# Performance work log

Hardware: AMD Instinct MI355X
Metric: run time of the kernel (lower is better)

## Reference

```python
import jax, jax.numpy as jnp
import numpy as np

H = W = 224
NSR = NSC = 8          # num_segments_row / col
BW = 5                 # band_width (default of adjust_boundaries)
K = NSR * NSC          # 64 superpixels
B = 256


def find_paths(g, inits, bw):
    """Seam-carving DP along axis 0 of g. g: (L, M); inits: (P,) start columns.
    Returns optimal paths (P, L) of column indices per row."""
    L, M = g.shape
    P = inits.shape[0]
    idx_pos = jnp.clip(inits[:, None] + jnp.arange(-bw, bw + 1)[None, :], 0, M - 1)  # (P, Np)
    Np = idx_pos.shape[1]
    C = -g[:, idx_pos]  # (L, P, Np) unary cost per row
    neigh = jnp.clip(jnp.arange(Np)[:, None] + jnp.array([-1, 0, 1])[None, :], 0, Np - 1)  # (Np,3)
    pos = jnp.arange(Np)
    r = jnp.arange(P)

    def step(cost_prev, c_y):
        padded = jnp.pad(cost_prev, ((0, 0), (1, 1)), constant_values=jnp.inf)  # (P, Np+2)
        prev_costs = padded[:, neigh + 1]                                        # (P, Np, 3)
        min_prev = prev_costs.min(axis=-1)
        min_idx = prev_costs.argmin(axis=-1)          # first-min, matches torch .min
        path_y = neigh[pos[None, :], min_idx]          # (P, Np) backpointers
        return min_prev + c_y, path_y

    cost_last, path_arr = jax.lax.scan(step, C[0], C[1:])  # path_arr: (L-1, P, Np)
    idx = jnp.argmin(cost_last, axis=1)                    # (P,)

    def back(idx, p_y):
        out = idx_pos[r, idx]
        return p_y[r, idx], out

    idx0, outs = jax.lax.scan(back, idx, path_arr, reverse=True)  # outs: (L-1, P) for y=1..L-1
    out0 = idx_pos[r, idx0]
    paths = jnp.concatenate([out0[None], outs], axis=0)  # (L, P)
    return paths.T


def segment_image(g):
    """g: (H, W) gradient map -> (H, W) int32 segmentation labels."""
    x_inits = jnp.clip(jnp.arange(1, NSC) * (W // NSC), 0, W - 1)
    y_inits = jnp.clip(jnp.arange(1, NSR) * (H // NSR), 0, H - 1)
    vpaths = find_paths(g, x_inits, BW)      # (7, H): column index per row
    hpaths = find_paths(g.T, y_inits, BW)    # (7, W): row index per column
    rows = jnp.broadcast_to(jnp.arange(H), vpaths.shape)
    cols = jnp.broadcast_to(jnp.arange(W), hpaths.shape)
    vmask = jnp.zeros((H, W), jnp.int32).at[rows, vpaths].set(1)
    hmask = jnp.zeros((H, W), jnp.int32).at[hpaths, cols].set(1)
    vlab = jnp.cumsum(vmask, axis=1)   # vertical label in [0, 7]
    hlab = jnp.cumsum(hmask, axis=0)   # horizontal label in [0, 7]
    return vlab + NSC * hlab           # labels in [0, 63]


def centroids_of(mask):
    flat = mask.reshape(-1)
    yc = jnp.repeat(jnp.arange(H, dtype=jnp.float32), W)
    xc = jnp.tile(jnp.arange(W, dtype=jnp.float32), H)
    sy = jax.ops.segment_sum(yc, flat, num_segments=K)
    sx = jax.ops.segment_sum(xc, flat, num_segments=K)
    cnt = jnp.maximum(jax.ops.segment_sum(jnp.ones_like(yc), flat, num_segments=K), 1e-6)
    return jnp.stack([sy / cnt, sx / cnt], axis=-1)  # (K, 2) [y, x]


def setup_inputs() -> dict:
    key = jax.random.key(0)
    k1, k2 = jax.random.split(key)
    x = jax.random.normal(k1, (B, 3, H, W), dtype=jnp.float32)
    grad_map = jax.random.uniform(k2, (B, H, W), dtype=jnp.float32)
    return {"x": x, "grad_map": grad_map}


def reference(x, grad_map):
    masks = jax.vmap(segment_image)(grad_map)          # (B, H, W) int32
    cents = jax.vmap(centroids_of)(masks)              # (B, K, 2) float32
    return cents, masks.astype(jnp.int64)
```

## Files before the change

### kernel.cpp

```cpp
#include <hip/hip_runtime.h>
#include <stdint.h>

#define HH 224
#define WW 224
#define NSEAM 7
#define BWIDTH 5
#define BB 256
#define KK 64
#define YCH 8
#define YROWS (HH / YCH)

#define DPPF_OLD(old, src, ctrl) \
    __int_as_float(__builtin_amdgcn_update_dpp(__float_as_int(old), __float_as_int(src), ctrl, 0xF, 0xF, false))
#define DPPF_Z(src, ctrl) \
    __int_as_float(__builtin_amdgcn_update_dpp(0, __float_as_int(src), ctrl, 0xF, 0xF, true))
#define DPPI_Z(src, ctrl) \
    __builtin_amdgcn_update_dpp(0, (int)(src), ctrl, 0xF, 0xF, true)

__global__ __launch_bounds__(256) void dp_kernel(const float* __restrict__ g,
                                                 int* __restrict__ paths,
                                                 unsigned long long* __restrict__ gacc) {
    __shared__ uint32_t ch[16][226];
    __shared__ int      pth[16][226];

    {
        int t = blockIdx.x * 256 + threadIdx.x;
        if (t < BB * KK) gacc[t] = 0ull;
    }

    const int j   = threadIdx.x & 15;
    const int grp = threadIdx.x >> 4;
    const int gid = blockIdx.x * 16 + grp;
    const int dir = gid / (BB * NSEAM);
    const int rem = gid - dir * (BB * NSEAM);
    const int b   = rem / NSEAM;
    const int p   = rem - b * NSEAM;
    const int band0 = 28 * (p + 1) - BWIDTH;
    const int jc  = (j > 10) ? 10 : j;
    const float* gb  = g + (size_t)b * HH * WW;
    const float* gp0 = gb + band0 + jc;
    const float* gp1 = gb + (size_t)(band0 + jc) * WW;
    const unsigned isj0 = (j == 0) ? 1u : 0u;

    float bufA[16], bufB[16], cost;

#define LOADC(BUF, c)                                                       \
    if (dir == 0) {                                                         \
        _Pragma("unroll")                                                   \
        for (int rr = 0; rr < 16; ++rr) BUF[rr] = gp0[((c) * 16 + rr) * WW];\
    } else {                                                                \
        const float4* q4 = reinterpret_cast<const float4*>(gp1 + (c) * 16); \
        float4 t0 = q4[0], t1 = q4[1], t2 = q4[2], t3 = q4[3];              \
        BUF[0] = t0.x;  BUF[1] = t0.y;  BUF[2] = t0.z;  BUF[3] = t0.w;      \
        BUF[4] = t1.x;  BUF[5] = t1.y;  BUF[6] = t1.z;  BUF[7] = t1.w;      \
        BUF[8] = t2.x;  BUF[9] = t2.y;  BUF[10] = t2.z; BUF[11] = t2.w;     \
        BUF[12] = t3.x; BUF[13] = t3.y; BUF[14] = t3.z; BUF[15] = t3.w;     \
    }

#define ROWSEL(BUF, rr)                                                     \
    {                                                                       \
        float pm  = DPPF_OLD(cost, cost, 0x111);                            \
        float pv  = DPPF_OLD(cost, cost, 0x101);                            \
        pv = (j >= 10) ? cost : pv;                                         \
        float best = fminf(fminf(pm, cost), pv);                            \
        unsigned cc = (cost == best) ? 1u : 0u;                             \
        unsigned b0 = (pm == best) ? isj0 : cc;                             \
        unsigned b1 = (pm == best) ? 0u : (cc ^ 1u);                        \
        cost = best - (BUF)[rr];                                            \
        selLo |= b0 << (rr);                                                \
        selHi |= b1 << (rr);                                                \
    }

#define TR16(x)                                                             \
    {                                                                       \
        unsigned pp;                                                        \
        pp = (unsigned)__builtin_amdgcn_ds_swizzle((int)(x), 0x201F);       \
        x = (j & 8) ? ((x & 0xFF00u) | ((pp >> 8) & 0x00FFu))               \
                    : ((x & 0x00FFu) | ((pp << 8) & 0xFF00u));              \
        pp = (unsigned)__builtin_amdgcn_ds_swizzle((int)(x), 0x101F);       \
        x = (j & 4) ? ((x & 0xF0F0u) | ((pp >> 4) & 0x0F0Fu))               \
                    : ((x & 0x0F0Fu) | ((pp << 4) & 0xF0F0u));              \
        pp = (unsigned)__builtin_amdgcn_ds_swizzle((int)(x), 0x081F);       \
        x = (j & 2) ? ((x & 0xCCCCu) | ((pp >> 2) & 0x3333u))               \
                    : ((x & 0x3333u) | ((pp << 2) & 0xCCCCu));              \
        pp = (unsigned)__builtin_amdgcn_ds_swizzle((int)(x), 0x041F);       \
        x = (j & 1) ? ((x & 0xAAAAu) | ((pp >> 1) & 0x5555u))               \
                    : ((x & 0x5555u) | ((pp << 1) & 0xAAAAu));              \
    }

#define PROCC(BUF, c)                                                       \
    {                                                                       \
        unsigned selLo = 0u, selHi = 0u;                                    \
        _Pragma("unroll")                                                   \
        for (int rr = 0; rr < 16; ++rr) ROWSEL(BUF, rr)                     \
        TR16(selLo)                                                         \
        TR16(selHi)                                                         \
        ch[grp][(c) * 16 + j] = selLo | (selHi << 16);                      \
    }

    LOADC(bufA, 0);
    LOADC(bufB, 1);
    {
        unsigned selLo = 0u, selHi = 0u;
        cost = -bufA[0];
#pragma unroll
        for (int rr = 1; rr < 16; ++rr) ROWSEL(bufA, rr)
        TR16(selLo)
        TR16(selHi)
        ch[grp][j] = selLo | (selHi << 16);
    }
    LOADC(bufA, 2);
    PROCC(bufB, 1);
    LOADC(bufB, 3);

#pragma unroll 1
    for (int c2 = 2; c2 <= 12; c2 += 2) {
        PROCC(bufA, c2);
        if (c2 + 2 < 14) LOADC(bufA, c2 + 2);
        PROCC(bufB, c2 + 1);
        if (c2 + 3 < 14) LOADC(bufB, c2 + 3);
    }

    float rc = (j <= 10) ? cost : INFINITY;
    int   ri = (j <= 10) ? j : 15;
#define REDSTEP(ctrl)                                                        \
    {                                                                        \
        float oc = DPPF_Z(rc, ctrl);                                         \
        int   oi = DPPI_Z(ri, ctrl);                                         \
        bool t = (oc < rc) || (oc == rc && oi < ri);                         \
        rc = t ? oc : rc; ri = t ? oi : ri;                                  \
    }
    REDSTEP(0x128) REDSTEP(0x124) REDSTEP(0x122) REDSTEP(0x121)
#undef REDSTEP

    int pos = ri;
    if (j == 0) pth[grp][HH - 1] = band0 + pos;

#pragma unroll 1
    for (int c = 13; c >= 0; --c) {
        uint32_t w[16];
#pragma unroll
        for (int rr = 0; rr < 16; ++rr) w[rr] = ch[grp][c * 16 + rr];
#pragma unroll
        for (int rr = 15; rr >= 0; --rr) {
            int r = c * 16 + rr;
            if (r >= 1) {
                uint32_t ww = w[rr];
                int sel = (int)((ww >> pos) & 1u) | (int)((ww >> (pos + 15)) & 2u);
                pos += sel - 1;
                if (j == 0) pth[grp][r - 1] = band0 + pos;
            }
        }
    }

    int* op = paths + (size_t)(b * 14 + dir * NSEAM + p) * HH;
#pragma unroll 1
    for (int c = 0; c < 14; ++c) op[c * 16 + j] = pth[grp][c * 16 + j];

#undef LOADC
#undef ROWSEL
#undef TR16
#undef PROCC
}

__global__ __launch_bounds__(256) void label_kernel(const int* __restrict__ paths,
                                                    float* __restrict__ out,
                                                    unsigned long long* __restrict__ gacc) {
    const int b  = blockIdx.x >> 3;
    const int cy = blockIdx.x & 7;
    const int y0 = cy * YROWS;

    __shared__ unsigned char vpc[NSEAM][YROWS];
    __shared__ unsigned long long acc[KK];

    const int* pb = paths + (size_t)b * 14 * HH;
    for (int i = threadIdx.x; i < NSEAM * YROWS; i += 256) {
        int q = i / YROWS, r = i - q * YROWS;
        vpc[q][r] = (unsigned char)pb[q * HH + y0 + r];
    }
    if (threadIdx.x < KK) acc[threadIdx.x] = 0ull;
    __syncthreads();

    const int x = threadIdx.x;
    if (x < WW) {
        int basev = 0, kv = 0, inv = 0;
        if (x >= 23) {
            int q = x - 23, k = q / 28, r = q - k * 28;
            if (k > 6) basev = 7;
            else { inv = (r <= 10) ? 1 : 0; basev = k + (r > 10 ? 1 : 0); kv = k; }
        }
        const int hA = (cy >= 1) ? pb[(NSEAM + cy - 1) * HH + x] : 0;
        const int hB = (cy <= 6) ? pb[(NSEAM + cy) * HH + x] : 0;

        float* mb = out + (size_t)BB * KK * 2 + (size_t)b * HH * WW + x;
        int cur = -1, ys = y0;

#define FLUSH(yend)                                                          \
        {                                                                    \
            unsigned cnt = (unsigned)((yend) - ys);                          \
            unsigned sy  = (unsigned)((ys + (yend) - 1) * ((yend) - ys) / 2);\
            unsigned sx  = (unsigned)x * cnt;                                \
            atomicAdd(&acc[cur], ((unsigned long long)cnt << 42) |           \
                                 ((unsigned long long)sy << 21) |            \
                                 (unsigned long long)sx);                    \
        }
#define ROW(t, HLEXPR)                                                       \
        {                                                                    \
            const int y = y0 + (t);                                          \
            int vl = basev + ((inv && (int)vpc[kv][t] <= x) ? 1 : 0);        \
            int lab = vl + 8 * (HLEXPR);                                     \
            mb[y * WW] = (float)lab;                                         \
            if (lab != cur) { if (cur >= 0) FLUSH(y); cur = lab; ys = y; }   \
        }
#pragma unroll
        for (int t = 0; t < 6; ++t)
            ROW(t, (cy >= 1) ? (cy - 1 + ((hA <= y0 + t) ? 1 : 0)) : 0)
#pragma unroll
        for (int t = 6; t < 23; ++t)
            ROW(t, cy)
#pragma unroll
        for (int t = 23; t < 28; ++t)
            ROW(t, (cy <= 6) ? (cy + ((hB <= y0 + t) ? 1 : 0)) : 7)
        FLUSH(y0 + YROWS)
#undef ROW
#undef FLUSH
    }
    __syncthreads();

    if (threadIdx.x < KK) {
        unsigned long long v = acc[threadIdx.x];
        if (v) atomicAdd(&gacc[(size_t)b * KK + threadIdx.x], v);
    }
}

__global__ __launch_bounds__(256) void finalize_kernel(const unsigned long long* __restrict__ gacc,
                                                       float* __restrict__ out) {
    int i = blockIdx.x * 256 + threadIdx.x;
    unsigned long long sv = gacc[i];
    float cnt = (float)(unsigned)(sv >> 42);
    float sy  = (float)(unsigned)((sv >> 21) & 0x1FFFFFu);
    float sx  = (float)(unsigned)(sv & 0x1FFFFFu);
    float c = fmaxf(cnt, 1e-6f);
    float2 r; r.x = sy / c; r.y = sx / c;
    *reinterpret_cast<float2*>(out + (size_t)i * 2) = r;
}

extern "C" void kernel_launch(void* const* d_in, const int* in_sizes, int n_in,
                              void* d_out, int out_size, void* d_ws, size_t ws_size,
                              hipStream_t stream) {
    const float* g = (const float*)d_in[1];
    float* out = (float*)d_out;
    int* paths = (int*)d_ws;
    unsigned long long* gacc =
        (unsigned long long*)((char*)d_ws + (size_t)BB * 14 * HH * 4);

    dp_kernel<<<(BB * 14) / 16, 256, 0, stream>>>(g, paths, gacc);
    label_kernel<<<BB * YCH, 256, 0, stream>>>(paths, out, gacc);
    finalize_kernel<<<(BB * KK) / 256, 256, 0, stream>>>(gacc, out);
}
```

Before: 45.52 us.

## Fuse DP, labeling and centroid finalize into one per-image kernel

Replaces three launches (seam DP, label/atomic accumulation, finalize) with one 1024-thread block per image. Seam paths stay in shared memory as bytes, and centroids are finalized from shared accumulators, so the global paths buffer, global atomics and two launches go away. In exchange only 256 blocks run, and during the DP phase just 224 of the 1024 threads are busy while the rest wait at the barrier. This cuts parallelism compared with the previous 224-block DP plus 2048-block label grid.

```diff
diff --git a/kernel.cpp b/kernel.cpp
--- a/kernel.cpp
+++ b/kernel.cpp
@@ -7,8 +7,6 @@
 #define BWIDTH 5
 #define BB 256
 #define KK 64
-#define YCH 8
-#define YROWS (HH / YCH)
 
 #define DPPF_OLD(old, src, ctrl) \
     __int_as_float(__builtin_amdgcn_update_dpp(__float_as_int(old), __float_as_int(src), ctrl, 0xF, 0xF, false))
@@ -17,32 +15,30 @@
 #define DPPI_Z(src, ctrl) \
     __builtin_amdgcn_update_dpp(0, (int)(src), ctrl, 0xF, 0xF, true)
 
-__global__ __launch_bounds__(256) void dp_kernel(const float* __restrict__ g,
-                                                 int* __restrict__ paths,
-                                                 unsigned long long* __restrict__ gacc) {
-    __shared__ uint32_t ch[16][226];
-    __shared__ int      pth[16][226];
-
-    {
-        int t = blockIdx.x * 256 + threadIdx.x;
-        if (t < BB * KK) gacc[t] = 0ull;
-    }
-
-    const int j   = threadIdx.x & 15;
-    const int grp = threadIdx.x >> 4;
-    const int gid = blockIdx.x * 16 + grp;
-    const int dir = gid / (BB * NSEAM);
-    const int rem = gid - dir * (BB * NSEAM);
-    const int b   = rem / NSEAM;
-    const int p   = rem - b * NSEAM;
-    const int band0 = 28 * (p + 1) - BWIDTH;
-    const int jc  = (j > 10) ? 10 : j;
-    const float* gb  = g + (size_t)b * HH * WW;
-    const float* gp0 = gb + band0 + jc;
-    const float* gp1 = gb + (size_t)(band0 + jc) * WW;
-    const unsigned isj0 = (j == 0) ? 1u : 0u;
-
-    float bufA[16], bufB[16], cost;
+__global__ __launch_bounds__(1024) void fused_kernel(const float* __restrict__ g,
+                                                     float* __restrict__ out) {
+    __shared__ uint32_t ch[14][226];
+    __shared__ unsigned char pv8[HH][8];
+    __shared__ unsigned char ph8[8][HH];
+    __shared__ unsigned long long acc[KK];
+
+    const int tid = threadIdx.x;
+    const int b   = blockIdx.x;
+    if (tid < KK) acc[tid] = 0ull;
+
+    if (tid < 14 * 16) {
+        const int j    = tid & 15;
+        const int grp  = tid >> 4;
+        const int dir  = grp / 7;
+        const int p    = grp % 7;
+        const int band0 = 28 * (p + 1) - BWIDTH;
+        const int jc   = (j > 10) ? 10 : j;
+        const float* gb  = g + (size_t)b * HH * WW;
+        const float* gp0 = gb + band0 + jc;
+        const float* gp1 = gb + (size_t)(band0 + jc) * WW;
+        const unsigned isj0 = (j == 0) ? 1u : 0u;
+
+        float bufA[16], bufB[16], cost;
 
 #define LOADC(BUF, c)                                                       \
     if (dir == 0) {                                                         \
@@ -98,90 +94,76 @@
         ch[grp][(c) * 16 + j] = selLo | (selHi << 16);                      \
     }
 
-    LOADC(bufA, 0);
-    LOADC(bufB, 1);
-    {
-        unsigned selLo = 0u, selHi = 0u;
-        cost = -bufA[0];
-#pragma unroll
-        for (int rr = 1; rr < 16; ++rr) ROWSEL(bufA, rr)
-        TR16(selLo)
-        TR16(selHi)
-        ch[grp][j] = selLo | (selHi << 16);
-    }
-    LOADC(bufA, 2);
-    PROCC(bufB, 1);
-    LOADC(bufB, 3);
+        LOADC(bufA, 0);
+        LOADC(bufB, 1);
+        {
+            unsigned selLo = 0u, selHi = 0u;
+            cost = -bufA[0];
+#pragma unroll
+            for (int rr = 1; rr < 16; ++rr) ROWSEL(bufA, rr)
+            TR16(selLo)
+            TR16(selHi)
+            ch[grp][j] = selLo | (selHi << 16);
+        }
+        LOADC(bufA, 2);
+        PROCC(bufB, 1);
+        LOADC(bufB, 3);
 
 #pragma unroll 1
-    for (int c2 = 2; c2 <= 12; c2 += 2) {
-        PROCC(bufA, c2);
-        if (c2 + 2 < 14) LOADC(bufA, c2 + 2);
-        PROCC(bufB, c2 + 1);
-        if (c2 + 3 < 14) LOADC(bufB, c2 + 3);
-    }
-
-    float rc = (j <= 10) ? cost : INFINITY;
-    int   ri = (j <= 10) ? j : 15;
+        for (int c2 = 2; c2 <= 12; c2 += 2) {
+            PROCC(bufA, c2);
+            if (c2 + 2 < 14) LOADC(bufA, c2 + 2);
+            PROCC(bufB, c2 + 1);
+            if (c2 + 3 < 14) LOADC(bufB, c2 + 3);
+        }
+
+        float rc = (j <= 10) ? cost : INFINITY;
+        int   ri = (j <= 10) ? j : 15;
 #define REDSTEP(ctrl)                                                        \
-    {                                                                        \
-        float oc = DPPF_Z(rc, ctrl);                                         \
-        int   oi = DPPI_Z(ri, ctrl);                                         \
-        bool t = (oc < rc) || (oc == rc && oi < ri);                         \
-        rc = t ? oc : rc; ri = t ? oi : ri;                                  \
-    }
-    REDSTEP(0x128) REDSTEP(0x124) REDSTEP(0x122) REDSTEP(0x121)
+        {                                                                    \
+            float oc = DPPF_Z(rc, ctrl);                                     \
+            int   oi = DPPI_Z(ri, ctrl);                                     \
+            bool t = (oc < rc) || (oc == rc && oi < ri);                     \
+            rc = t ? oc : rc; ri = t ? oi : ri;                              \
+        }
+        REDSTEP(0x128) REDSTEP(0x124) REDSTEP(0x122) REDSTEP(0x121)
 #undef REDSTEP
 
-    int pos = ri;
-    if (j == 0) pth[grp][HH - 1] = band0 + pos;
+        int pos = ri;
+        const bool wr = (j == 0);
+        if (wr) {
+            if (dir == 0) pv8[HH - 1][p] = (unsigned char)(band0 + pos);
+            else          ph8[p][HH - 1] = (unsigned char)(band0 + pos);
+        }
 
 #pragma unroll 1
-    for (int c = 13; c >= 0; --c) {
-        uint32_t w[16];
-#pragma unroll
-        for (int rr = 0; rr < 16; ++rr) w[rr] = ch[grp][c * 16 + rr];
-#pragma unroll
-        for (int rr = 15; rr >= 0; --rr) {
-            int r = c * 16 + rr;
-            if (r >= 1) {
-                uint32_t ww = w[rr];
-                int sel = (int)((ww >> pos) & 1u) | (int)((ww >> (pos + 15)) & 2u);
-                pos += sel - 1;
-                if (j == 0) pth[grp][r - 1] = band0 + pos;
+        for (int c = 13; c >= 0; --c) {
+            uint32_t w[16];
+#pragma unroll
+            for (int rr = 0; rr < 16; ++rr) w[rr] = ch[grp][c * 16 + rr];
+#pragma unroll
+            for (int rr = 15; rr >= 0; --rr) {
+                int r = c * 16 + rr;
+                if (r >= 1) {
+                    uint32_t ww = w[rr];
+                    int sel = (int)((ww >> pos) & 1u) | (int)((ww >> (pos + 15)) & 2u);
+                    pos += sel - 1;
+                    if (wr) {
+                        if (dir == 0) pv8[r - 1][p] = (unsigned char)(band0 + pos);
+                        else          ph8[p][r - 1] = (unsigned char)(band0 + pos);
+                    }
+                }
             }
         }
-    }
-
-    int* op = paths + (size_t)(b * 14 + dir * NSEAM + p) * HH;
-#pragma unroll 1
-    for (int c = 0; c < 14; ++c) op[c * 16 + j] = pth[grp][c * 16 + j];
-
 #undef LOADC
 #undef ROWSEL
 #undef TR16
 #undef PROCC
-}
-
-__global__ __launch_bounds__(256) void label_kernel(const int* __restrict__ paths,
-                                                    float* __restrict__ out,
-                                                    unsigned long long* __restrict__ gacc) {
-    const int b  = blockIdx.x >> 3;
-    const int cy = blockIdx.x & 7;
-    const int y0 = cy * YROWS;
-
-    __shared__ unsigned char vpc[NSEAM][YROWS];
-    __shared__ unsigned long long acc[KK];
-
-    const int* pb = paths + (size_t)b * 14 * HH;
-    for (int i = threadIdx.x; i < NSEAM * YROWS; i += 256) {
-        int q = i / YROWS, r = i - q * YROWS;
-        vpc[q][r] = (unsigned char)pb[q * HH + y0 + r];
-    }
-    if (threadIdx.x < KK) acc[threadIdx.x] = 0ull;
+    }
+
     __syncthreads();
 
-    const int x = threadIdx.x;
+    const int x = tid & 255;
     if (x < WW) {
         int basev = 0, kv = 0, inv = 0;
         if (x >= 23) {
@@ -189,60 +171,58 @@
             if (k > 6) basev = 7;
             else { inv = (r <= 10) ? 1 : 0; basev = k + (r > 10 ? 1 : 0); kv = k; }
         }
-        const int hA = (cy >= 1) ? pb[(NSEAM + cy - 1) * HH + x] : 0;
-        const int hB = (cy <= 6) ? pb[(NSEAM + cy) * HH + x] : 0;
-
         float* mb = out + (size_t)BB * KK * 2 + (size_t)b * HH * WW + x;
-        int cur = -1, ys = y0;
+
+#pragma unroll
+        for (int ov = 0; ov < 2; ++ov) {
+            const int cy = (tid >> 8) + 4 * ov;
+            const int y0 = cy * 28;
+            const int hA = (cy >= 1) ? (int)ph8[cy - 1][x] : 0;
+            const int hB = (cy <= 6) ? (int)ph8[cy][x] : 0;
+            int cur = -1, ys = y0;
 
 #define FLUSH(yend)                                                          \
-        {                                                                    \
-            unsigned cnt = (unsigned)((yend) - ys);                          \
-            unsigned sy  = (unsigned)((ys + (yend) - 1) * ((yend) - ys) / 2);\
-            unsigned sx  = (unsigned)x * cnt;                                \
-            atomicAdd(&acc[cur], ((unsigned long long)cnt << 42) |           \
-                                 ((unsigned long long)sy << 21) |            \
-                                 (unsigned long long)sx);                    \
-        }
+            {                                                                \
+                unsigned cnt = (unsigned)((yend) - ys);                      \
+                unsigned sy  = (unsigned)((ys + (yend) - 1) * ((yend) - ys) / 2);\
+                unsigned sx  = (unsigned)x * cnt;                            \
+                atomicAdd(&acc[cur], ((unsigned long long)cnt << 42) |       \
+                                     ((unsigned long long)sy << 21) |        \
+                                     (unsigned long long)sx);                \
+            }
 #define ROW(t, HLEXPR)                                                       \
-        {                                                                    \
-            const int y = y0 + (t);                                          \
-            int vl = basev + ((inv && (int)vpc[kv][t] <= x) ? 1 : 0);        \
-            int lab = vl + 8 * (HLEXPR);                                     \
-            mb[y * WW] = (float)lab;                                         \
-            if (lab != cur) { if (cur >= 0) FLUSH(y); cur = lab; ys = y; }   \
-        }
-#pragma unroll
-        for (int t = 0; t < 6; ++t)
-            ROW(t, (cy >= 1) ? (cy - 1 + ((hA <= y0 + t) ? 1 : 0)) : 0)
-#pragma unroll
-        for (int t = 6; t < 23; ++t)
-            ROW(t, cy)
-#pragma unroll
-        for (int t = 23; t < 28; ++t)
-            ROW(t, (cy <= 6) ? (cy + ((hB <= y0 + t) ? 1 : 0)) : 7)
-        FLUSH(y0 + YROWS)
+            {                                                                \
+                const int y = y0 + (t);                                      \
+                int vl = basev + ((inv && (int)pv8[y][kv] <= x) ? 1 : 0);    \
+                int lab = vl + 8 * (HLEXPR);                                 \
+                mb[y * WW] = (float)lab;                                     \
+                if (lab != cur) { if (cur >= 0) FLUSH(y); cur = lab; ys = y; }\
+            }
+#pragma unroll
+            for (int t = 0; t < 6; ++t)
+                ROW(t, (cy >= 1) ? (cy - 1 + ((hA <= y0 + t) ? 1 : 0)) : 0)
+#pragma unroll
+            for (int t = 6; t < 23; ++t)
+                ROW(t, cy)
+#pragma unroll
+            for (int t = 23; t < 28; ++t)
+                ROW(t, (cy <= 6) ? (cy + ((hB <= y0 + t) ? 1 : 0)) : 7)
+            FLUSH(y0 + 28)
 #undef ROW
 #undef FLUSH
+        }
     }
     __syncthreads();
 
-    if (threadIdx.x < KK) {
-        unsigned long long v = acc[threadIdx.x];
-        if (v) atomicAdd(&gacc[(size_t)b * KK + threadIdx.x], v);
-    }
-}
-
-__global__ __launch_bounds__(256) void finalize_kernel(const unsigned long long* __restrict__ gacc,
-                                                       float* __restrict__ out) {
-    int i = blockIdx.x * 256 + threadIdx.x;
-    unsigned long long sv = gacc[i];
-    float cnt = (float)(unsigned)(sv >> 42);
-    float sy  = (float)(unsigned)((sv >> 21) & 0x1FFFFFu);
-    float sx  = (float)(unsigned)(sv & 0x1FFFFFu);
-    float c = fmaxf(cnt, 1e-6f);
-    float2 r; r.x = sy / c; r.y = sx / c;
-    *reinterpret_cast<float2*>(out + (size_t)i * 2) = r;
+    if (tid < KK) {
+        unsigned long long sv = acc[tid];
+        float cnt = (float)(unsigned)(sv >> 42);
+        float sy  = (float)(unsigned)((sv >> 21) & 0x1FFFFFu);
+        float sx  = (float)(unsigned)(sv & 0x1FFFFFu);
+        float c = fmaxf(cnt, 1e-6f);
+        float2 r; r.x = sy / c; r.y = sx / c;
+        *reinterpret_cast<float2*>(out + (size_t)b * KK * 2 + tid * 2) = r;
+    }
 }
 
 extern "C" void kernel_launch(void* const* d_in, const int* in_sizes, int n_in,
@@ -250,11 +230,5 @@
                               hipStream_t stream) {
     const float* g = (const float*)d_in[1];
     float* out = (float*)d_out;
-    int* paths = (int*)d_ws;
-    unsigned long long* gacc =
-        (unsigned long long*)((char*)d_ws + (size_t)BB * 14 * HH * 4);
-
-    dp_kernel<<<(BB * 14) / 16, 256, 0, stream>>>(g, paths, gacc);
-    label_kernel<<<BB * YCH, 256, 0, stream>>>(paths, out, gacc);
-    finalize_kernel<<<(BB * KK) / 256, 256, 0, stream>>>(gacc, out);
+    fused_kernel<<<BB, 1024, 0, stream>>>(g, out);
 }
```

Result: slower. 49.00 us (+7.6%).
